# Kernel optimization log

Measured on AMD Instinct MI355X. Metric: run time of the kernel, lower is better.

The kernel has to match this reference:

```python
import jax, jax.numpy as jnp
import numpy as np
from jax import lax

MOTIF_DIM = 283
HIDDEN = 256
DEPTH = 7
KPROF = 20


def _conv1d(h, w, b, dilation, pad):
    # h: (N, C, L), w: (O, I, K)
    y = lax.conv_general_dilated(h, w, window_strides=(1,), padding=[pad],
                                 rhs_dilation=(dilation,),
                                 dimension_numbers=('NCH', 'OIH', 'NCH'))
    return y + b[None, :, None]


def setup_inputs() -> dict:
    key = jax.random.key(0)
    ks = jax.random.split(key, 10)
    batch, n_peak, chunk_len = 2, 128, 512
    L = n_peak * chunk_len
    s = lambda fan: 1.0 / np.sqrt(fan)
    x = jax.random.normal(ks[0], (batch, L, MOTIF_DIM), dtype=jnp.float32)
    w_proj = jax.random.normal(ks[1], (HIDDEN, MOTIF_DIM), dtype=jnp.float32) * s(MOTIF_DIM)
    tower_w = jax.random.normal(ks[2], (DEPTH, HIDDEN, HIDDEN, 3), dtype=jnp.float32) * s(HIDDEN * 3)
    tower_b = jax.random.normal(ks[3], (DEPTH, HIDDEN), dtype=jnp.float32) * 0.01
    w_prof = jax.random.normal(ks[4], (1, HIDDEN, KPROF), dtype=jnp.float32) * s(HIDDEN * KPROF)
    b_prof = jax.random.normal(ks[5], (1,), dtype=jnp.float32) * 0.01
    w_atpm = jax.random.normal(ks[6], (1, HIDDEN, 1), dtype=jnp.float32) * s(HIDDEN)
    b_atpm = jax.random.normal(ks[7], (1,), dtype=jnp.float32) * 0.01
    n_peaks = jax.random.randint(ks[8], (batch,), 0, n_peak).astype(jnp.int64)
    return {"x": x, "w_proj": w_proj, "tower_w": tower_w, "tower_b": tower_b,
            "w_prof": w_prof, "b_prof": b_prof, "w_atpm": w_atpm, "b_atpm": b_atpm,
            "n_peaks": n_peaks, "peak_split": chunk_len, "max_n_peaks": n_peak}


def reference(x, w_proj, tower_w, tower_b, w_prof, b_prof, w_atpm, b_atpm,
              n_peaks, peak_split, max_n_peaks):
    batch, L, _ = x.shape
    chunk_len = peak_split
    # motif_proj: pointwise conv == linear projection
    h = jnp.einsum('blm,hm->blh', x, w_proj)                       # (B, L, H)
    # split concatenated padded peaks into uniform windows
    h = h.reshape(batch * max_n_peaks, chunk_len, HIDDEN)
    h = jnp.transpose(h, (0, 2, 1))                                 # (N, H, Lc)
    # dilated conv tower: dilation 2^(i+1), same length; h = gelu(c) + c
    for i in range(DEPTH):
        d = 2 ** (i + 1)
        c = _conv1d(h, tower_w[i], tower_b[i], d, (d, d))
        h = jax.nn.gelu(c, approximate=False) + c
    # profile header: kernel 20, torch 'same' padding -> (9, 10)
    profile = _conv1d(h, w_prof, b_prof, 1, (9, 10))                # (N, 1, Lc)
    # mean pool over length, then atpm header (1x1 conv over hidden)
    pooled = h.mean(axis=2)                                         # (N, H)
    atpm = pooled @ w_atpm[0, :, 0] + b_atpm[0]                     # (N,)
    atpm = atpm.reshape(batch, max_n_peaks)
    mask = jnp.arange(max_n_peaks)[None, :] < n_peaks[:, None]
    peak_atpms = jnp.where(mask, atpm, 0.0)                         # (B, P)
    peak_profiles = profile[:, 0, :].reshape(batch, max_n_peaks, chunk_len)
    return peak_atpms, peak_profiles
```

## Files before the change

### kernel.cpp

```cpp
#include <hip/hip_runtime.h>
#include <hip/hip_bf16.h>
#include <math.h>

#define MOTIF  283
#define KPAD   288
#define HIDDEN 256
#define DEPTH  7
#define KPROF  20
#define CHUNK  512
#define NCHUNK 256
#define NTOK   131072
#define BK     32

using bf16 = __hip_bfloat16;
typedef short bf16x8 __attribute__((ext_vector_type(8)));
typedef float f32x4  __attribute__((ext_vector_type(4)));

#define GLD_LDS(g, l) __builtin_amdgcn_global_load_lds( \
    (const __attribute__((address_space(1))) void*)(g), \
    (__attribute__((address_space(3))) void*)(l), 16, 0, 0)

__device__ __forceinline__ float gelu_res(float c){
  return 0.5f * c * (1.0f + erff(c * 0.70710678118654752f)) + c;
}

__global__ __launch_bounds__(256) void k_prep_tower(
    const float* __restrict__ w, bf16* __restrict__ wt){
  const int idx = blockIdx.x * 256 + threadIdx.x;
  if (idx < DEPTH * 3 * HIDDEN * HIDDEN){
    const int ci = idx & 255;
    const int co = (idx >> 8) & 255;
    const int lt = idx >> 16;
    const int layer = lt / 3, tap = lt % 3;
    wt[idx] = __float2bfloat16(
        w[(((size_t)layer * HIDDEN + co) * HIDDEN + ci) * 3 + tap]);
  }
}

__global__ __launch_bounds__(256) void k_prep_wproj(
    const float* __restrict__ w, bf16* __restrict__ wt){
  const int idx = blockIdx.x * 256 + threadIdx.x;
  if (idx < HIDDEN * KPAD){
    const int co = idx / KPAD, m = idx % KPAD;
    wt[idx] = __float2bfloat16(m < MOTIF ? w[(size_t)co * MOTIF + m] : 0.0f);
  }
}

__global__ __launch_bounds__(256) void k_prep_whead(
    const float* __restrict__ wprof, const float* __restrict__ watpm,
    bf16* __restrict__ wh, bf16* __restrict__ zp){
  const int idx = blockIdx.x * 256 + threadIdx.x;
  if (idx < 2048) zp[idx] = __float2bfloat16(0.0f);
  if (idx < 32 * 256){
    const int k = idx >> 8, ci = idx & 255;
    float v = 0.0f;
    if (k < KPROF) v = wprof[ci * KPROF + k];
    else if (k == KPROF) v = watpm[ci];
    wh[idx] = __float2bfloat16(v);
  }
}

__global__ __launch_bounds__(256, 3) void k_proj(
    const float* __restrict__ x, const bf16* __restrict__ wprojT,
    bf16* __restrict__ h0){
  __shared__ __align__(16) bf16 Xs[64 * KPAD];
  const int t0  = blockIdx.x * 64;
  const int tid = threadIdx.x;
  const int wid = tid >> 6, lane = tid & 63;
  const int lr = lane & 15, kq = lane >> 4;
  const int cow = wid * 64;

  for (int r = wid; r < 64; r += 4){
    const float* xrow = x + (size_t)(t0 + r) * MOTIF;
    #pragma unroll
    for (int mi = 0; mi < 5; ++mi){
      const int m = lane + mi * 64;
      if (m < KPAD)
        Xs[r * KPAD + m] = __float2bfloat16(m < MOTIF ? xrow[m] : 0.0f);
    }
  }
  __syncthreads();

  f32x4 acc[4][4];
  #pragma unroll
  for (int mt = 0; mt < 4; ++mt)
    #pragma unroll
    for (int nt = 0; nt < 4; ++nt) acc[mt][nt] = (f32x4){0.f, 0.f, 0.f, 0.f};

  for (int m0 = 0; m0 < KPAD; m0 += BK){
    bf16x8 a[4], b[4];
    #pragma unroll
    for (int mt = 0; mt < 4; ++mt)
      a[mt] = *(const bf16x8*)(
          wprojT + (size_t)(cow + mt * 16 + lr) * KPAD + m0 + kq * 8);
    #pragma unroll
    for (int nt = 0; nt < 4; ++nt)
      b[nt] = *(const bf16x8*)(Xs + (nt * 16 + lr) * KPAD + m0 + kq * 8);
    #pragma unroll
    for (int mt = 0; mt < 4; ++mt)
      #pragma unroll
      for (int nt = 0; nt < 4; ++nt)
        acc[mt][nt] = __builtin_amdgcn_mfma_f32_16x16x32_bf16(
            a[mt], b[nt], acc[mt][nt], 0, 0, 0);
  }

  #pragma unroll
  for (int mt = 0; mt < 4; ++mt){
    const int co = cow + mt * 16 + kq * 4;
    #pragma unroll
    for (int nt = 0; nt < 4; ++nt){
      const int tok = t0 + nt * 16 + lr;
      bf16 ov[4];
      #pragma unroll
      for (int r = 0; r < 4; ++r) ov[r] = __float2bfloat16(acc[mt][nt][r]);
      *(uint2*)(h0 + (size_t)tok * HIDDEN + co) = *(uint2*)ov;
    }
  }
}

__global__ __launch_bounds__(256, 3) void k_conv(
    const bf16* __restrict__ hin, bf16* __restrict__ hout,
    const bf16* __restrict__ wl,
    const float* __restrict__ bias, const bf16* __restrict__ zp, int dil){
  __shared__ __align__(16) bf16 As[3 * 128 * BK];
  __shared__ __align__(16) bf16 Bs[3 * 128 * BK];
  const int n   = blockIdx.z;
  const int co0 = blockIdx.y * 128;
  const int l0  = blockIdx.x * 128;
  const int tid = threadIdx.x;
  const int wid = tid >> 6, lane = tid & 63;
  const int lr = lane & 15, kq = lane >> 4;
  const int mw = wid & 1, nw = wid >> 1;

  const bf16* hbase = hin + (size_t)n * CHUNK * HIDDEN;

  const bf16* gA[6]; const bf16* gB[6]; int stepB[6];
  #pragma unroll
  for (int j = 0; j < 6; ++j){
    const int i   = j * 256 + tid;
    const int row = i >> 2, c = i & 3;
    const int cc  = c ^ (row & 3);
    const int tap = row >> 7;
    const int r   = row & 127;
    gA[j] = wl + ((size_t)(tap * 256 + co0 + r) << 8) + cc * 8;
    const int l = l0 + r + (tap - 1) * dil;
    const bool v = (unsigned)l < CHUNK;
    gB[j] = v ? hbase + ((size_t)l << 8) + cc * 8 : zp + ((i & 255) * 8);
    stepB[j] = v ? BK : 0;
  }

  f32x4 acc[4][4];
  #pragma unroll
  for (int mt = 0; mt < 4; ++mt)
    #pragma unroll
    for (int nt = 0; nt < 4; ++nt) acc[mt][nt] = (f32x4){0.f, 0.f, 0.f, 0.f};

  const int sw = (kq ^ (lr & 3)) << 3;
  const bf16* Ab = As + (mw * 64 + lr) * BK + sw;
  const bf16* Bb = Bs + (nw * 64 + lr) * BK + sw;

  const bool do0 = (l0 + 127 - dil) >= 0;
  const bool do2 = (l0 + dil) < CHUNK;

  for (int it = 0; it < HIDDEN / BK; ++it){
    __syncthreads();
    #pragma unroll
    for (int j = 0; j < 6; ++j){
      GLD_LDS(gA[j], As + (j * 256 + wid * 64) * 8);
      GLD_LDS(gB[j], Bs + (j * 256 + wid * 64) * 8);
    }
    __syncthreads();

    #pragma unroll
    for (int t = 0; t < 3; ++t){
      if (t == 0 && !do0) continue;
      if (t == 2 && !do2) continue;
      bf16x8 a[4], b[4];
      #pragma unroll
      for (int mt = 0; mt < 4; ++mt)
        a[mt] = *(const bf16x8*)(Ab + t * 4096 + mt * 512);
      #pragma unroll
      for (int nt = 0; nt < 4; ++nt)
        b[nt] = *(const bf16x8*)(Bb + t * 4096 + nt * 512);
      #pragma unroll
      for (int mt = 0; mt < 4; ++mt)
        #pragma unroll
        for (int nt = 0; nt < 4; ++nt)
          acc[mt][nt] = __builtin_amdgcn_mfma_f32_16x16x32_bf16(
              a[mt], b[nt], acc[mt][nt], 0, 0, 0);
    }

    #pragma unroll
    for (int j = 0; j < 6; ++j){ gA[j] += BK; gB[j] += stepB[j]; }
  }

  bf16* obase = hout + (size_t)n * CHUNK * HIDDEN;
  #pragma unroll
  for (int mt = 0; mt < 4; ++mt){
    const int co = co0 + mw * 64 + mt * 16 + kq * 4;
    const float b0 = bias[co], b1 = bias[co + 1];
    const float b2 = bias[co + 2], b3 = bias[co + 3];
    #pragma unroll
    for (int nt = 0; nt < 4; ++nt){
      const int l = l0 + nw * 64 + nt * 16 + lr;
      bf16 ov[4];
      ov[0] = __float2bfloat16(gelu_res(acc[mt][nt][0] + b0));
      ov[1] = __float2bfloat16(gelu_res(acc[mt][nt][1] + b1));
      ov[2] = __float2bfloat16(gelu_res(acc[mt][nt][2] + b2));
      ov[3] = __float2bfloat16(gelu_res(acc[mt][nt][3] + b3));
      *(uint2*)(obase + (size_t)l * HIDDEN + co) = *(uint2*)ov;
    }
  }
}

__global__ __launch_bounds__(256, 2) void k_head(
    const bf16* __restrict__ h, const bf16* __restrict__ wheadT,
    float* __restrict__ PT){
  __shared__ __align__(16) bf16 Xs[128 * BK];
  __shared__ __align__(16) bf16 Wh[32 * 256];
  const int t0 = blockIdx.x * 128;
  const int tid = threadIdx.x;
  const int wid = tid >> 6, lane = tid & 63;
  const int lr = lane & 15, kq = lane >> 4;
  const int mw = wid & 1, nw = wid >> 1;

  for (int i = tid; i < 1024; i += 256)
    ((uint4*)Wh)[i] = ((const uint4*)wheadT)[i];

  f32x4 acc[4];
  #pragma unroll
  for (int mt = 0; mt < 4; ++mt) acc[mt] = (f32x4){0.f, 0.f, 0.f, 0.f};

  for (int ci0 = 0; ci0 < HIDDEN; ci0 += BK){
    __syncthreads();
    for (int i = tid; i < 512; i += 256){
      const int row = i >> 2, q = i & 3;
      *(uint4*)(Xs + row * BK + q * 8) =
          *(const uint4*)(h + (size_t)(t0 + row) * HIDDEN + ci0 + q * 8);
    }
    __syncthreads();
    const bf16x8 b = *(const bf16x8*)(Wh + (nw * 16 + lr) * 256 + ci0 + kq * 8);
    #pragma unroll
    for (int mt = 0; mt < 4; ++mt){
      const bf16x8 a = *(const bf16x8*)(Xs + (mw * 64 + mt * 16 + lr) * BK + kq * 8);
      acc[mt] = __builtin_amdgcn_mfma_f32_16x16x32_bf16(a, b, acc[mt], 0, 0, 0);
    }
  }
  const int k_out = nw * 16 + lr;
  #pragma unroll
  for (int mt = 0; mt < 4; ++mt){
    const int tok = t0 + mw * 64 + mt * 16 + kq * 4;
    *(f32x4*)(PT + (size_t)k_out * NTOK + tok) = acc[mt];
  }
}

__global__ __launch_bounds__(256) void k_combine(
    const float* __restrict__ PT, const float* __restrict__ bprof,
    float* __restrict__ out){
  const int t = blockIdx.x * 256 + threadIdx.x;
  const int n = t >> 9, l = t & 511;
  float acc = bprof[0];
  const float* base = PT + ((size_t)n << 9);
  #pragma unroll
  for (int k = 0; k < KPROF; ++k){
    const int j = l + k - 9;
    if ((unsigned)j < CHUNK) acc += base[(size_t)k * NTOK + j];
  }
  out[NCHUNK + t] = acc;
}

__global__ __launch_bounds__(256) void k_atpm(
    const float* __restrict__ PT, const float* __restrict__ batpm,
    const int* __restrict__ n_peaks, float* __restrict__ out){
  __shared__ float red[4];
  const int n = blockIdx.x, tid = threadIdx.x;
  const float* row = PT + (size_t)KPROF * NTOK + ((size_t)n << 9);
  float p = row[tid] + row[tid + 256];
  #pragma unroll
  for (int off = 32; off > 0; off >>= 1) p += __shfl_down(p, off, 64);
  if ((tid & 63) == 0) red[tid >> 6] = p;
  __syncthreads();
  if (tid == 0){
    const float s = red[0] + red[1] + red[2] + red[3];
    const float a = s * (1.0f / 512.0f) + batpm[0];
    out[n] = ((n & 127) < n_peaks[n >> 7]) ? a : 0.0f;
  }
}

extern "C" void kernel_launch(void* const* d_in, const int* in_sizes, int n_in,
                              void* d_out, int out_size, void* d_ws, size_t ws_size,
                              hipStream_t stream){
  const float* x       = (const float*)d_in[0];
  const float* w_proj  = (const float*)d_in[1];
  const float* tower_w = (const float*)d_in[2];
  const float* tower_b = (const float*)d_in[3];
  const float* w_prof  = (const float*)d_in[4];
  const float* b_prof  = (const float*)d_in[5];
  const float* w_atpm  = (const float*)d_in[6];
  const float* b_atpm  = (const float*)d_in[7];
  const int*   n_peaks = (const int*)d_in[8];
  float* out = (float*)d_out;

  char* ws = (char*)d_ws;
  bf16*  h0     = (bf16*)ws;
  bf16*  h1     = (bf16*)(ws + 67108864);
  float* PT     = (float*)(ws + 134217728);
  bf16*  wtowT  = (bf16*)(ws + 150994944);
  bf16*  wheadT = (bf16*)(ws + 153747456);
  bf16*  wprojT = (bf16*)(ws + 153763840);
  bf16*  zp     = (bf16*)(ws + 153911296);

  k_prep_tower<<<5376, 256, 0, stream>>>(tower_w, wtowT);
  k_prep_wproj<<<(HIDDEN * KPAD + 255) / 256, 256, 0, stream>>>(w_proj, wprojT);
  k_prep_whead<<<32, 256, 0, stream>>>(w_prof, w_atpm, wheadT, zp);

  k_proj<<<NTOK / 64, 256, 0, stream>>>(x, wprojT, h0);

  bf16* cur = h0; bf16* nxt = h1;
  for (int i = 0; i < DEPTH; ++i){
    k_conv<<<dim3(CHUNK / 128, 2, NCHUNK), 256, 0, stream>>>(
        cur, nxt, wtowT + (size_t)i * 3 * HIDDEN * HIDDEN,
        tower_b + i * HIDDEN, zp, 2 << i);
    bf16* t = cur; cur = nxt; nxt = t;
  }

  k_head<<<1024, 256, 0, stream>>>(cur, wheadT, PT);
  k_combine<<<512, 256, 0, stream>>>(PT, b_prof, out);
  k_atpm<<<256, 256, 0, stream>>>(PT, b_atpm, n_peaks, out);
}
```

Before: 946.9 us.

## Retile projection GEMM into 128x128 blocks with K-stepped swizzled LDS staging

Reworks the motif projection kernel from 64-token blocks that stage the whole x tile and read weights straight from global memory into 128x128 (channel x token) tiles. Each K-step of 32 loads weights via global_load_lds and x rows into XOR-swizzled LDS buffers. This shrinks LDS use so more blocks fit per CU, and it moves weight reads out of uncoalesced per-lane global loads. In exchange, every x row is now read twice (once per channel half), and each K-step adds two barriers with no double buffering.

```diff
diff --git a/kernel.cpp b/kernel.cpp
--- a/kernel.cpp
+++ b/kernel.cpp
@@ -60,26 +60,31 @@
   }
 }
 
-__global__ __launch_bounds__(256, 3) void k_proj(
+__global__ __launch_bounds__(256, 4) void k_proj(
     const float* __restrict__ x, const bf16* __restrict__ wprojT,
     bf16* __restrict__ h0){
-  __shared__ __align__(16) bf16 Xs[64 * KPAD];
-  const int t0  = blockIdx.x * 64;
+  __shared__ __align__(16) bf16 As[128 * BK];
+  __shared__ __align__(16) bf16 Bs[128 * BK];
+  const int t0  = blockIdx.x * 128;
+  const int co0 = blockIdx.y * 128;
   const int tid = threadIdx.x;
   const int wid = tid >> 6, lane = tid & 63;
   const int lr = lane & 15, kq = lane >> 4;
-  const int cow = wid * 64;
-
-  for (int r = wid; r < 64; r += 4){
-    const float* xrow = x + (size_t)(t0 + r) * MOTIF;
-    #pragma unroll
-    for (int mi = 0; mi < 5; ++mi){
-      const int m = lane + mi * 64;
-      if (m < KPAD)
-        Xs[r * KPAD + m] = __float2bfloat16(m < MOTIF ? xrow[m] : 0.0f);
-    }
-  }
-  __syncthreads();
+  const int mw = wid & 1, nw = wid >> 1;
+
+  const bf16* gA[2];
+  #pragma unroll
+  for (int j = 0; j < 2; ++j){
+    const int i   = j * 256 + tid;
+    const int row = i >> 2, c = i & 3;
+    const int cc  = c ^ (row & 3);
+    gA[j] = wprojT + (size_t)(co0 + row) * KPAD + cc * 8;
+  }
+
+  const int brow = tid >> 1, bhalf = tid & 1;
+  const float* xrow = x + (size_t)(t0 + brow) * MOTIF;
+  bf16* bdst0 = Bs + brow * BK + (((bhalf * 2)     ^ (brow & 3)) << 3);
+  bf16* bdst1 = Bs + brow * BK + (((bhalf * 2 + 1) ^ (brow & 3)) << 3);
 
   f32x4 acc[4][4];
   #pragma unroll
@@ -87,15 +92,37 @@
     #pragma unroll
     for (int nt = 0; nt < 4; ++nt) acc[mt][nt] = (f32x4){0.f, 0.f, 0.f, 0.f};
 
+  const int sw = (kq ^ (lr & 3)) << 3;
+  const bf16* Ab = As + (mw * 64 + lr) * BK + sw;
+  const bf16* Bb = Bs + (nw * 64 + lr) * BK + sw;
+
   for (int m0 = 0; m0 < KPAD; m0 += BK){
+    __syncthreads();
+    GLD_LDS(gA[0], As + (wid * 64) * 8);
+    GLD_LDS(gA[1], As + (256 + wid * 64) * 8);
+    gA[0] += BK; gA[1] += BK;
+
+    bf16 ov[16];
+    const int mbase = m0 + bhalf * 16;
+    if (m0 + BK <= MOTIF){
+      #pragma unroll
+      for (int e = 0; e < 16; ++e) ov[e] = __float2bfloat16(xrow[mbase + e]);
+    } else {
+      #pragma unroll
+      for (int e = 0; e < 16; ++e){
+        const int m = mbase + e;
+        ov[e] = __float2bfloat16(m < MOTIF ? xrow[m] : 0.0f);
+      }
+    }
+    *(uint4*)bdst0 = *(uint4*)(ov);
+    *(uint4*)bdst1 = *(uint4*)(ov + 8);
+    __syncthreads();
+
     bf16x8 a[4], b[4];
     #pragma unroll
-    for (int mt = 0; mt < 4; ++mt)
-      a[mt] = *(const bf16x8*)(
-          wprojT + (size_t)(cow + mt * 16 + lr) * KPAD + m0 + kq * 8);
-    #pragma unroll
-    for (int nt = 0; nt < 4; ++nt)
-      b[nt] = *(const bf16x8*)(Xs + (nt * 16 + lr) * KPAD + m0 + kq * 8);
+    for (int mt = 0; mt < 4; ++mt) a[mt] = *(const bf16x8*)(Ab + mt * 512);
+    #pragma unroll
+    for (int nt = 0; nt < 4; ++nt) b[nt] = *(const bf16x8*)(Bb + nt * 512);
     #pragma unroll
     for (int mt = 0; mt < 4; ++mt)
       #pragma unroll
@@ -106,10 +133,10 @@
 
   #pragma unroll
   for (int mt = 0; mt < 4; ++mt){
-    const int co = cow + mt * 16 + kq * 4;
+    const int co = co0 + mw * 64 + mt * 16 + kq * 4;
     #pragma unroll
     for (int nt = 0; nt < 4; ++nt){
-      const int tok = t0 + nt * 16 + lr;
+      const int tok = t0 + nw * 64 + nt * 16 + lr;
       bf16 ov[4];
       #pragma unroll
       for (int r = 0; r < 4; ++r) ov[r] = __float2bfloat16(acc[mt][nt][r]);
@@ -314,7 +341,7 @@
   k_prep_wproj<<<(HIDDEN * KPAD + 255) / 256, 256, 0, stream>>>(w_proj, wprojT);
   k_prep_whead<<<32, 256, 0, stream>>>(w_prof, w_atpm, wheadT, zp);
 
-  k_proj<<<NTOK / 64, 256, 0, stream>>>(x, wprojT, h0);
+  k_proj<<<dim3(NTOK / 128, 2), 256, 0, stream>>>(x, wprojT, h0);
 
   bf16* cur = h0; bf16* nxt = h1;
   for (int i = 0; i < DEPTH; ++i){
```

New measurement: 969.7 us. +2.4%, slower.
